# Performance work log

Measured on AMD Instinct MI355X. Metric: run time of the kernel, lower is better.

Reference implementation:

```python
import jax, jax.numpy as jnp
import numpy as np

N_NODES = 100000
N_EDGES = 1600000
N_GRAPHS = 1024
IN_DIM = 7
HID = 64
OUT = 64
BN_EPS = 1e-5


def setup_inputs() -> dict:
    key = jax.random.key(0)
    ks = jax.random.split(key, 20)
    x = jax.random.normal(ks[0], (N_NODES, IN_DIM), dtype=jnp.float32)
    edge_index = jax.random.randint(ks[1], (2, N_EDGES), 0, N_NODES, dtype=jnp.int32)
    batch = jnp.sort(jax.random.randint(ks[2], (N_NODES,), 0, N_GRAPHS, dtype=jnp.int32))
    d = {"x": x, "edge_index": edge_index, "batch": batch}
    dims = [(IN_DIM, HID), (HID, HID), (HID, HID)]
    for l, (din, dout) in enumerate(dims):
        k = jax.random.split(ks[3 + l], 4)
        d[f"w1_l{l}"] = jax.random.normal(k[0], (din, dout), dtype=jnp.float32) / np.sqrt(din)
        d[f"b1_l{l}"] = jnp.zeros((dout,), dtype=jnp.float32)
        d[f"w2_l{l}"] = jax.random.normal(k[1], (dout, dout), dtype=jnp.float32) / np.sqrt(dout)
        d[f"b2_l{l}"] = jnp.zeros((dout,), dtype=jnp.float32)
        d[f"gamma_l{l}"] = jnp.ones((dout,), dtype=jnp.float32)
        d[f"beta_l{l}"] = jnp.zeros((dout,), dtype=jnp.float32)
    d["proj_w"] = jax.random.normal(ks[10], (HID, OUT), dtype=jnp.float32) / np.sqrt(HID)
    d["proj_b"] = jnp.zeros((OUT,), dtype=jnp.float32)
    return d


def _gin_layer(x, src, dst, w1, b1, w2, b2, gamma, beta):
    # GINConv (eps=0): h_i = MLP(x_i + sum_{j->i} x_j)
    agg = jax.ops.segment_sum(x[src], dst, num_segments=N_NODES) + x
    h = jnp.dot(jax.nn.relu(jnp.dot(agg, w1) + b1), w2) + b2
    # BatchNorm1d, training-mode batch statistics
    mean = h.mean(axis=0)
    var = h.var(axis=0)
    h = (h - mean) * jax.lax.rsqrt(var + BN_EPS) * gamma + beta
    return jax.nn.relu(h)


def reference(x, edge_index, batch,
              w1_l0, b1_l0, w2_l0, b2_l0, gamma_l0, beta_l0,
              w1_l1, b1_l1, w2_l1, b2_l1, gamma_l1, beta_l1,
              w1_l2, b1_l2, w2_l2, b2_l2, gamma_l2, beta_l2,
              proj_w, proj_b):
    src, dst = edge_index[0], edge_index[1]
    layers = [
        (w1_l0, b1_l0, w2_l0, b2_l0, gamma_l0, beta_l0),
        (w1_l1, b1_l1, w2_l1, b2_l1, gamma_l1, beta_l1),
        (w1_l2, b1_l2, w2_l2, b2_l2, gamma_l2, beta_l2),
    ]
    h = x
    for (w1, b1, w2, b2, g, be) in layers:
        h = _gin_layer(h, src, dst, w1, b1, w2, b2, g, be)
    # global mean pool over graphs
    sums = jax.ops.segment_sum(h, batch, num_segments=N_GRAPHS)
    counts = jax.ops.segment_sum(jnp.ones((N_NODES,), dtype=h.dtype), batch, num_segments=N_GRAPHS)
    pooled = sums / jnp.maximum(counts, 1.0)[:, None]
    out = jnp.dot(pooled, proj_w) + proj_b
    norm = jnp.linalg.norm(out, axis=-1, keepdims=True)
    return out / jnp.maximum(norm, 1e-12)
```

## Files before the change

kernel.cpp:

```cpp
#include <hip/hip_runtime.h>

#define N_NODES 100000
#define N_EDGES 1600000
#define N_GRAPHS 1024
#define BN_EPS 1e-5f
#define BSH 6
#define BNODES 64
#define NBUCK 1563
#define NB 128
#define CH 12500
#define MS_N (NBUCK * NB)
#define MS_SBLK ((MS_N + 1023) / 1024)

__global__ __launch_bounds__(256) void msplit_hist(const int* __restrict__ dst,
                                                   int* __restrict__ hist_g) {
    __shared__ int lh[NBUCK];
    for (int i = threadIdx.x; i < NBUCK; i += 256) lh[i] = 0;
    __syncthreads();
    int e0 = blockIdx.x * CH;
    int e1 = min(e0 + CH, N_EDGES);
    for (int e = e0 + threadIdx.x; e < e1; e += 256)
        atomicAdd(&lh[dst[e] >> BSH], 1);
    __syncthreads();
    for (int i = threadIdx.x; i < NBUCK; i += 256)
        hist_g[i * NB + blockIdx.x] = lh[i];
}

__global__ __launch_bounds__(256) void ms_scan_blocks(const int* __restrict__ in,
                                                      int* __restrict__ out,
                                                      int* __restrict__ bsum) {
    __shared__ int ts[256];
    int base = blockIdx.x * 1024 + threadIdx.x * 4;
    int c[4];
#pragma unroll
    for (int i = 0; i < 4; i++) {
        int idx = base + i;
        c[i] = (idx < MS_N) ? in[idx] : 0;
    }
    int s = c[0] + c[1] + c[2] + c[3];
    ts[threadIdx.x] = s;
    __syncthreads();
    for (int off = 1; off < 256; off <<= 1) {
        int v = (threadIdx.x >= off) ? ts[threadIdx.x - off] : 0;
        __syncthreads();
        ts[threadIdx.x] += v;
        __syncthreads();
    }
    int run = ts[threadIdx.x] - s;
#pragma unroll
    for (int i = 0; i < 4; i++) {
        int idx = base + i;
        if (idx < MS_N) out[idx] = run;
        run += c[i];
    }
    if (threadIdx.x == 255) bsum[blockIdx.x] = ts[255];
}

__global__ void ms_scan_sums(int* bsum) {
    if (threadIdx.x == 0) {
        int run = 0;
        for (int i = 0; i < MS_SBLK; i++) {
            int v = bsum[i];
            bsum[i] = run;
            run += v;
        }
    }
}

__global__ __launch_bounds__(256) void ms_scan_apply(int* __restrict__ data,
                                                     const int* __restrict__ bsum,
                                                     int* __restrict__ bptr) {
    int i = blockIdx.x * 256 + threadIdx.x;
    if (i < MS_N) {
        int v = data[i] + bsum[i >> 10];
        data[i] = v;
        if ((i & (NB - 1)) == 0) bptr[i / NB] = v;
    }
    if (i == 0) bptr[NBUCK] = N_EDGES;
}

__global__ __launch_bounds__(256) void msplit_place(const int* __restrict__ src,
                                                    const int* __restrict__ dst,
                                                    const int* __restrict__ hist_s,
                                                    int* __restrict__ ebuf) {
    __shared__ int lbase[NBUCK];
    for (int i = threadIdx.x; i < NBUCK; i += 256)
        lbase[i] = hist_s[i * NB + blockIdx.x];
    __syncthreads();
    int e0 = blockIdx.x * CH;
    int e1 = min(e0 + CH, N_EDGES);
    for (int e = e0 + threadIdx.x; e < e1; e += 256) {
        int d = dst[e];
        int p = atomicAdd(&lbase[d >> BSH], 1);
        ebuf[p] = ((d & (BNODES - 1)) << 17) | src[e];
    }
}

__global__ __launch_bounds__(256) void bucket_csr(const int* __restrict__ ebuf,
                                                  const int* __restrict__ bptr,
                                                  int* __restrict__ rowptr,
                                                  int* __restrict__ cnt,
                                                  int* __restrict__ elist) {
    int b = blockIdx.x;
    int rs = bptr[b], re = bptr[b + 1];
    int nbase = b << BSH;
    __shared__ int lcnt[BNODES], loff[BNODES];
    if (threadIdx.x < BNODES) lcnt[threadIdx.x] = 0;
    __syncthreads();
    for (int i = rs + threadIdx.x; i < re; i += 256)
        atomicAdd(&lcnt[ebuf[i] >> 17], 1);
    __syncthreads();
    if (threadIdx.x < BNODES) loff[threadIdx.x] = lcnt[threadIdx.x];
    __syncthreads();
    for (int off = 1; off < BNODES; off <<= 1) {
        int v = 0;
        if (threadIdx.x < BNODES && threadIdx.x >= off) v = loff[threadIdx.x - off];
        __syncthreads();
        if (threadIdx.x < BNODES) loff[threadIdx.x] += v;
        __syncthreads();
    }
    if (threadIdx.x < BNODES) {
        loff[threadIdx.x] -= lcnt[threadIdx.x];
        int n = nbase + threadIdx.x;
        if (n < N_NODES) {
            rowptr[n] = rs + loff[threadIdx.x];
            cnt[n] = lcnt[threadIdx.x];
        }
    }
    __syncthreads();
    for (int i = rs + threadIdx.x; i < re; i += 256) {
        int pk = ebuf[i];
        int p = atomicAdd(&loff[pk >> 17], 1);
        elist[rs + p] = pk & 0x1FFFF;
    }
}

__global__ __launch_bounds__(256) void gbounds(const int* __restrict__ batch,
                                               int* __restrict__ grow) {
    int g = blockIdx.x * 256 + threadIdx.x;
    if (g > N_GRAPHS) return;
    int lo = 0, hi = N_NODES;
    while (lo < hi) {
        int mid = (lo + hi) >> 1;
        if (batch[mid] < g) lo = mid + 1;
        else hi = mid;
    }
    grow[g] = lo;
}

__global__ __launch_bounds__(256) void gather7(const float* __restrict__ x,
                                               const int* __restrict__ rowptr,
                                               const int* __restrict__ cnt,
                                               const int* __restrict__ elist,
                                               float* __restrict__ agg) {
    int t = blockIdx.x * 256 + threadIdx.x;
    int n = t >> 3, f = t & 7;
    if (n >= N_NODES || f >= 7) return;
    int start = rowptr[n], k = cnt[n];
    float a = x[(size_t)n * 7 + f];
    for (int i = 0; i < k; i++) {
        int s = elist[start + i];
        a += x[(size_t)s * 7 + f];
    }
    agg[(size_t)n * 7 + f] = a;
}

__global__ __launch_bounds__(256) void gather64_bn(const float* __restrict__ h2,
                                                   const float* __restrict__ ss,
                                                   const int* __restrict__ rowptr,
                                                   const int* __restrict__ cnt,
                                                   const int* __restrict__ elist,
                                                   float* __restrict__ agg) {
    int t = blockIdx.x * 256 + threadIdx.x;
    int n = t >> 4, c = t & 15;
    if (n >= N_NODES) return;
    float4 sc = ((const float4*)ss)[c];
    float4 sh = ((const float4*)(ss + 64))[c];
    int start = rowptr[n], k = cnt[n];
    const float4* h4 = (const float4*)h2;
    float4 v = h4[(size_t)n * 16 + c];
    float4 a;
    a.x = fmaxf(fmaf(v.x, sc.x, sh.x), 0.0f);
    a.y = fmaxf(fmaf(v.y, sc.y, sh.y), 0.0f);
    a.z = fmaxf(fmaf(v.z, sc.z, sh.z), 0.0f);
    a.w = fmaxf(fmaf(v.w, sc.w, sh.w), 0.0f);
    for (int i = 0; i < k; i++) {
        int s = elist[start + i];
        float4 w = h4[(size_t)s * 16 + c];
        a.x += fmaxf(fmaf(w.x, sc.x, sh.x), 0.0f);
        a.y += fmaxf(fmaf(w.y, sc.y, sh.y), 0.0f);
        a.z += fmaxf(fmaf(w.z, sc.z, sh.z), 0.0f);
        a.w += fmaxf(fmaf(w.w, sc.w, sh.w), 0.0f);
    }
    ((float4*)agg)[(size_t)n * 16 + c] = a;
}

template <int DIN>
__global__ __launch_bounds__(256) void mlp_kernel(const float* __restrict__ agg,
                                                  const float* __restrict__ w1,
                                                  const float* __restrict__ b1,
                                                  const float* __restrict__ w2,
                                                  const float* __restrict__ b2,
                                                  float* __restrict__ h2out) {
    int row = blockIdx.x * 256 + threadIdx.x;
    if (row >= N_NODES) return;
    const float* xr = agg + (size_t)row * DIN;

    float h1[64];
#pragma unroll
    for (int j = 0; j < 64; j++) h1[j] = b1[j];

    if constexpr (DIN == 7) {
#pragma unroll
        for (int k = 0; k < 7; k++) {
            float xv = xr[k];
#pragma unroll
            for (int j = 0; j < 64; j++) h1[j] = fmaf(xv, w1[k * 64 + j], h1[j]);
        }
    } else {
        const float4* xp = (const float4*)xr;
        for (int kk = 0; kk < DIN / 4; kk++) {
            float4 xv = xp[kk];
            const float* w = w1 + kk * 4 * 64;
#pragma unroll
            for (int j = 0; j < 64; j++) h1[j] = fmaf(xv.x, w[j], h1[j]);
#pragma unroll
            for (int j = 0; j < 64; j++) h1[j] = fmaf(xv.y, w[64 + j], h1[j]);
#pragma unroll
            for (int j = 0; j < 64; j++) h1[j] = fmaf(xv.z, w[128 + j], h1[j]);
#pragma unroll
            for (int j = 0; j < 64; j++) h1[j] = fmaf(xv.w, w[192 + j], h1[j]);
        }
    }
#pragma unroll
    for (int j = 0; j < 64; j++) h1[j] = fmaxf(h1[j], 0.0f);

    for (int j4 = 0; j4 < 16; j4++) {
        float4 o;
        float* ov = (float*)&o;
#pragma unroll
        for (int jj = 0; jj < 4; jj++) {
            int j = j4 * 4 + jj;
            float a = b2[j];
#pragma unroll
            for (int k = 0; k < 64; k++) a = fmaf(h1[k], w2[k * 64 + j], a);
            ov[jj] = a;
        }
        ((float4*)(h2out + (size_t)row * 64))[j4] = o;
    }
}

__global__ __launch_bounds__(256) void bn_stats(const float* __restrict__ h2,
                                                double* __restrict__ acc) {
    long base = (long)blockIdx.x * 256 * 64;
    long end = base + 256L * 64;
    long lim = (long)N_NODES * 64;
    if (end > lim) end = lim;
    float s = 0.f, sq = 0.f;
    for (long i = base + threadIdx.x; i < end; i += 256) {
        float v = h2[i];
        s += v;
        sq += v * v;
    }
    __shared__ float ls[256], lq[256];
    ls[threadIdx.x] = s;
    lq[threadIdx.x] = sq;
    __syncthreads();
    if (threadIdx.x < 64) {
        float S = ls[threadIdx.x] + ls[threadIdx.x + 64] + ls[threadIdx.x + 128] + ls[threadIdx.x + 192];
        float Q = lq[threadIdx.x] + lq[threadIdx.x + 64] + lq[threadIdx.x + 128] + lq[threadIdx.x + 192];
        atomicAdd(&acc[threadIdx.x], (double)S);
        atomicAdd(&acc[64 + threadIdx.x], (double)Q);
    }
}

__global__ void bn_finalize(const double* __restrict__ acc, const float* __restrict__ gamma,
                            const float* __restrict__ beta, float* __restrict__ ss) {
    int j = threadIdx.x;
    if (j >= 64) return;
    double inv = 1.0 / (double)N_NODES;
    double mean = acc[j] * inv;
    double var = acc[64 + j] * inv - mean * mean;
    float scale = gamma[j] / sqrtf((float)var + BN_EPS);
    ss[j] = scale;
    ss[64 + j] = beta[j] - (float)mean * scale;
}

__global__ __launch_bounds__(256) void pool_bn(const float* __restrict__ h2,
                                               const float* __restrict__ ss,
                                               const int* __restrict__ grow,
                                               float* __restrict__ pooled) {
    int g = blockIdx.x;
    int start = grow[g], end = grow[g + 1];
    int c = threadIdx.x & 15, grp = threadIdx.x >> 4;
    float4 sc = ((const float4*)ss)[c];
    float4 sh = ((const float4*)(ss + 64))[c];
    const float4* h4 = (const float4*)h2;
    float4 a = {0.f, 0.f, 0.f, 0.f};
    for (int n = start + grp; n < end; n += 16) {
        float4 v = h4[(size_t)n * 16 + c];
        a.x += fmaxf(fmaf(v.x, sc.x, sh.x), 0.0f);
        a.y += fmaxf(fmaf(v.y, sc.y, sh.y), 0.0f);
        a.z += fmaxf(fmaf(v.z, sc.z, sh.z), 0.0f);
        a.w += fmaxf(fmaf(v.w, sc.w, sh.w), 0.0f);
    }
    __shared__ float4 ls[256];
    ls[threadIdx.x] = a;
    __syncthreads();
    for (int off = 128; off >= 16; off >>= 1) {
        if (threadIdx.x < off) {
            float4 b = ls[threadIdx.x + off];
            ls[threadIdx.x].x += b.x;
            ls[threadIdx.x].y += b.y;
            ls[threadIdx.x].z += b.z;
            ls[threadIdx.x].w += b.w;
        }
        __syncthreads();
    }
    if (threadIdx.x < 16) {
        float inv = 1.0f / fmaxf((float)(end - start), 1.0f);
        float4 r = ls[threadIdx.x];
        r.x *= inv; r.y *= inv; r.z *= inv; r.w *= inv;
        ((float4*)pooled)[(size_t)g * 16 + threadIdx.x] = r;
    }
}

__global__ __launch_bounds__(256) void final_proj(const float* __restrict__ pooled,
                                                  const float* __restrict__ pw,
                                                  const float* __restrict__ pb,
                                                  float* __restrict__ out) {
    __shared__ float sw[64 * 64];
    for (int i = threadIdx.x; i < 4096; i += 256) sw[i] = pw[i];
    __syncthreads();
    int g = blockIdx.x * 4 + (threadIdx.x >> 6);
    int j = threadIdx.x & 63;
    if (g >= N_GRAPHS) return;
    float a = pb[j];
#pragma unroll
    for (int k = 0; k < 64; k++) a = fmaf(pooled[(size_t)g * 64 + k], sw[k * 64 + j], a);
    float ss2 = a * a;
#pragma unroll
    for (int off = 1; off < 64; off <<= 1) ss2 += __shfl_xor(ss2, off);
    out[(size_t)g * 64 + j] = a / fmaxf(sqrtf(ss2), 1e-12f);
}

extern "C" void kernel_launch(void* const* d_in, const int* in_sizes, int n_in,
                              void* d_out, int out_size, void* d_ws, size_t ws_size,
                              hipStream_t stream) {
    const float* x = (const float*)d_in[0];
    const int* eidx = (const int*)d_in[1];
    const int* batch = (const int*)d_in[2];
    const int* src = eidx;
    const int* dst = eidx + N_EDGES;
    const float* W1[3] = {(const float*)d_in[3], (const float*)d_in[9], (const float*)d_in[15]};
    const float* B1[3] = {(const float*)d_in[4], (const float*)d_in[10], (const float*)d_in[16]};
    const float* W2[3] = {(const float*)d_in[5], (const float*)d_in[11], (const float*)d_in[17]};
    const float* B2[3] = {(const float*)d_in[6], (const float*)d_in[12], (const float*)d_in[18]};
    const float* GM[3] = {(const float*)d_in[7], (const float*)d_in[13], (const float*)d_in[19]};
    const float* BT[3] = {(const float*)d_in[8], (const float*)d_in[14], (const float*)d_in[20]};
    const float* PW = (const float*)d_in[21];
    const float* PB = (const float*)d_in[22];
    float* out = (float*)d_out;

    char* ws = (char*)d_ws;
    size_t off = 0;
    auto alloc = [&](size_t bytes) -> void* {
        void* p = ws + off;
        off += (bytes + 255) & ~(size_t)255;
        return p;
    };
    float* A    = (float*)alloc((size_t)N_NODES * 64 * 4);
    float* C    = (float*)alloc((size_t)N_NODES * 64 * 4);
    float* agg0 = (float*)alloc((size_t)N_NODES * 7 * 4);
    int* cnt    = (int*)alloc((size_t)N_NODES * 4);
    int* rowptr = (int*)alloc((size_t)N_NODES * 4);
    int* elist  = (int*)alloc((size_t)N_EDGES * 4);
    int* ebuf   = (int*)alloc((size_t)N_EDGES * 4);
    int* hist_g = (int*)alloc((size_t)MS_N * 4);
    int* hist_s = (int*)alloc((size_t)MS_N * 4);
    int* msum   = (int*)alloc((size_t)MS_SBLK * 4);
    int* bptr   = (int*)alloc((size_t)(NBUCK + 1) * 4);
    int* grow   = (int*)alloc(1025 * 4);
    double* acc = (double*)alloc(3 * 128 * sizeof(double));
    float* ss0    = (float*)alloc(128 * 4);
    float* ss1    = (float*)alloc(128 * 4);
    float* ss2    = (float*)alloc(128 * 4);
    float* pooled = (float*)alloc((size_t)N_GRAPHS * 64 * 4);

    hipMemsetAsync(acc, 0, 3 * 128 * sizeof(double), stream);

    const int row_grid = (N_NODES + 255) / 256;
    const int vec_grid = (N_NODES * 16 + 255) / 256;
    const int g7_grid = (N_NODES * 8 + 255) / 256;

    msplit_hist<<<NB, 256, 0, stream>>>(dst, hist_g);
    ms_scan_blocks<<<MS_SBLK, 256, 0, stream>>>(hist_g, hist_s, msum);
    ms_scan_sums<<<1, 64, 0, stream>>>(msum);
    ms_scan_apply<<<(MS_N + 255) / 256, 256, 0, stream>>>(hist_s, msum, bptr);
    msplit_place<<<NB, 256, 0, stream>>>(src, dst, hist_s, ebuf);
    bucket_csr<<<NBUCK, 256, 0, stream>>>(ebuf, bptr, rowptr, cnt, elist);
    gbounds<<<5, 256, 0, stream>>>(batch, grow);

    gather7<<<g7_grid, 256, 0, stream>>>(x, rowptr, cnt, elist, agg0);
    mlp_kernel<7><<<row_grid, 256, 0, stream>>>(agg0, W1[0], B1[0], W2[0], B2[0], A);
    bn_stats<<<row_grid, 256, 0, stream>>>(A, acc);
    bn_finalize<<<1, 64, 0, stream>>>(acc, GM[0], BT[0], ss0);

    gather64_bn<<<vec_grid, 256, 0, stream>>>(A, ss0, rowptr, cnt, elist, C);
    mlp_kernel<64><<<row_grid, 256, 0, stream>>>(C, W1[1], B1[1], W2[1], B2[1], A);
    bn_stats<<<row_grid, 256, 0, stream>>>(A, acc + 128);
    bn_finalize<<<1, 64, 0, stream>>>(acc + 128, GM[1], BT[1], ss1);

    gather64_bn<<<vec_grid, 256, 0, stream>>>(A, ss1, rowptr, cnt, elist, C);
    mlp_kernel<64><<<row_grid, 256, 0, stream>>>(C, W1[2], B1[2], W2[2], B2[2], A);
    bn_stats<<<row_grid, 256, 0, stream>>>(A, acc + 256);
    bn_finalize<<<1, 64, 0, stream>>>(acc + 256, GM[2], BT[2], ss2);

    pool_bn<<<N_GRAPHS, 256, 0, stream>>>(A, ss2, grow, pooled);

    final_proj<<<N_GRAPHS / 4, 256, 0, stream>>>(pooled, PW, PB, out);
}
```

Before: 558.8 us.

## Split neighbor gather across four lanes per feature chunk; pad x to 8

gather64_bn now assigns a full 64-lane wavefront per node, with four lane groups each summing a strided quarter of the neighbor list before a shuffle-xor reduction. This gives more parallelism per node and more loads in flight, which shortens the serial per-node edge loop. The first-layer input is padded to 8 floats so the gather reads aligned rows. The edge-split histogram also uses more blocks with smaller chunks. The cost is four times as many threads in the gather, an extra padding kernel and buffer, and a larger histogram scan.

```diff
diff --git a/kernel.cpp b/kernel.cpp
--- a/kernel.cpp
+++ b/kernel.cpp
@@ -7,8 +7,8 @@
 #define BSH 6
 #define BNODES 64
 #define NBUCK 1563
-#define NB 128
-#define CH 12500
+#define NB 256
+#define CH 6250
 #define MS_N (NBUCK * NB)
 #define MS_SBLK ((MS_N + 1023) / 1024)
 
@@ -148,21 +148,29 @@
     grow[g] = lo;
 }
 
-__global__ __launch_bounds__(256) void gather7(const float* __restrict__ x,
+__global__ __launch_bounds__(256) void pad8(const float* __restrict__ x,
+                                            float* __restrict__ x8) {
+    int t = blockIdx.x * 256 + threadIdx.x;
+    if (t >= N_NODES * 8) return;
+    int n = t >> 3, f = t & 7;
+    x8[t] = (f < 7) ? x[(size_t)n * 7 + f] : 0.0f;
+}
+
+__global__ __launch_bounds__(256) void gather7(const float* __restrict__ x8,
                                                const int* __restrict__ rowptr,
                                                const int* __restrict__ cnt,
                                                const int* __restrict__ elist,
                                                float* __restrict__ agg) {
     int t = blockIdx.x * 256 + threadIdx.x;
     int n = t >> 3, f = t & 7;
-    if (n >= N_NODES || f >= 7) return;
+    if (n >= N_NODES) return;
     int start = rowptr[n], k = cnt[n];
-    float a = x[(size_t)n * 7 + f];
+    float a = x8[(size_t)n * 8 + f];
     for (int i = 0; i < k; i++) {
         int s = elist[start + i];
-        a += x[(size_t)s * 7 + f];
-    }
-    agg[(size_t)n * 7 + f] = a;
+        a += x8[(size_t)s * 8 + f];
+    }
+    if (f < 7) agg[(size_t)n * 7 + f] = a;
 }
 
 __global__ __launch_bounds__(256) void gather64_bn(const float* __restrict__ h2,
@@ -172,19 +180,16 @@
                                                    const int* __restrict__ elist,
                                                    float* __restrict__ agg) {
     int t = blockIdx.x * 256 + threadIdx.x;
-    int n = t >> 4, c = t & 15;
+    int n = t >> 6;
     if (n >= N_NODES) return;
+    int l = t & 63;
+    int c = l & 15, q = l >> 4;
     float4 sc = ((const float4*)ss)[c];
     float4 sh = ((const float4*)(ss + 64))[c];
     int start = rowptr[n], k = cnt[n];
     const float4* h4 = (const float4*)h2;
-    float4 v = h4[(size_t)n * 16 + c];
-    float4 a;
-    a.x = fmaxf(fmaf(v.x, sc.x, sh.x), 0.0f);
-    a.y = fmaxf(fmaf(v.y, sc.y, sh.y), 0.0f);
-    a.z = fmaxf(fmaf(v.z, sc.z, sh.z), 0.0f);
-    a.w = fmaxf(fmaf(v.w, sc.w, sh.w), 0.0f);
-    for (int i = 0; i < k; i++) {
+    float4 a = {0.f, 0.f, 0.f, 0.f};
+    for (int i = q; i < k; i += 4) {
         int s = elist[start + i];
         float4 w = h4[(size_t)s * 16 + c];
         a.x += fmaxf(fmaf(w.x, sc.x, sh.x), 0.0f);
@@ -192,7 +197,18 @@
         a.z += fmaxf(fmaf(w.z, sc.z, sh.z), 0.0f);
         a.w += fmaxf(fmaf(w.w, sc.w, sh.w), 0.0f);
     }
-    ((float4*)agg)[(size_t)n * 16 + c] = a;
+    a.x += __shfl_xor(a.x, 16); a.y += __shfl_xor(a.y, 16);
+    a.z += __shfl_xor(a.z, 16); a.w += __shfl_xor(a.w, 16);
+    a.x += __shfl_xor(a.x, 32); a.y += __shfl_xor(a.y, 32);
+    a.z += __shfl_xor(a.z, 32); a.w += __shfl_xor(a.w, 32);
+    if (q == 0) {
+        float4 v = h4[(size_t)n * 16 + c];
+        a.x += fmaxf(fmaf(v.x, sc.x, sh.x), 0.0f);
+        a.y += fmaxf(fmaf(v.y, sc.y, sh.y), 0.0f);
+        a.z += fmaxf(fmaf(v.z, sc.z, sh.z), 0.0f);
+        a.w += fmaxf(fmaf(v.w, sc.w, sh.w), 0.0f);
+        ((float4*)agg)[(size_t)n * 16 + c] = a;
+    }
 }
 
 template <int DIN>
@@ -372,6 +388,7 @@
     float* A    = (float*)alloc((size_t)N_NODES * 64 * 4);
     float* C    = (float*)alloc((size_t)N_NODES * 64 * 4);
     float* agg0 = (float*)alloc((size_t)N_NODES * 7 * 4);
+    float* x8   = (float*)alloc((size_t)N_NODES * 8 * 4);
     int* cnt    = (int*)alloc((size_t)N_NODES * 4);
     int* rowptr = (int*)alloc((size_t)N_NODES * 4);
     int* elist  = (int*)alloc((size_t)N_EDGES * 4);
@@ -390,8 +407,8 @@
     hipMemsetAsync(acc, 0, 3 * 128 * sizeof(double), stream);
 
     const int row_grid = (N_NODES + 255) / 256;
-    const int vec_grid = (N_NODES * 16 + 255) / 256;
     const int g7_grid = (N_NODES * 8 + 255) / 256;
+    const int g64_grid = (N_NODES * 64 + 255) / 256;
 
     msplit_hist<<<NB, 256, 0, stream>>>(dst, hist_g);
     ms_scan_blocks<<<MS_SBLK, 256, 0, stream>>>(hist_g, hist_s, msum);
@@ -400,18 +417,19 @@
     msplit_place<<<NB, 256, 0, stream>>>(src, dst, hist_s, ebuf);
     bucket_csr<<<NBUCK, 256, 0, stream>>>(ebuf, bptr, rowptr, cnt, elist);
     gbounds<<<5, 256, 0, stream>>>(batch, grow);
-
-    gather7<<<g7_grid, 256, 0, stream>>>(x, rowptr, cnt, elist, agg0);
+    pad8<<<g7_grid, 256, 0, stream>>>(x, x8);
+
+    gather7<<<g7_grid, 256, 0, stream>>>(x8, rowptr, cnt, elist, agg0);
     mlp_kernel<7><<<row_grid, 256, 0, stream>>>(agg0, W1[0], B1[0], W2[0], B2[0], A);
     bn_stats<<<row_grid, 256, 0, stream>>>(A, acc);
     bn_finalize<<<1, 64, 0, stream>>>(acc, GM[0], BT[0], ss0);
 
-    gather64_bn<<<vec_grid, 256, 0, stream>>>(A, ss0, rowptr, cnt, elist, C);
+    gather64_bn<<<g64_grid, 256, 0, stream>>>(A, ss0, rowptr, cnt, elist, C);
     mlp_kernel<64><<<row_grid, 256, 0, stream>>>(C, W1[1], B1[1], W2[1], B2[1], A);
     bn_stats<<<row_grid, 256, 0, stream>>>(A, acc + 128);
     bn_finalize<<<1, 64, 0, stream>>>(acc + 128, GM[1], BT[1], ss1);
 
-    gather64_bn<<<vec_grid, 256, 0, stream>>>(A, ss1, rowptr, cnt, elist, C);
+    gather64_bn<<<g64_grid, 256, 0, stream>>>(A, ss1, rowptr, cnt, elist, C);
     mlp_kernel<64><<<row_grid, 256, 0, stream>>>(C, W1[2], B1[2], W2[2], B2[2], A);
     bn_stats<<<row_grid, 256, 0, stream>>>(A, acc + 256);
     bn_finalize<<<1, 64, 0, stream>>>(acc + 256, GM[2], BT[2], ss2);
```

Result: no change. 550.9 us (-1.4%).
